# Optimization experiments

Hardware: AMD Instinct MI355X
Metric: run time of the kernel (lower is better)

The kernel has to match this reference:

```python
import jax, jax.numpy as jnp
import numpy as np

EMBED_DIM = 1024
NUM_HEADS = 16
HEAD_DIM = EMBED_DIM // NUM_HEADS
STD = 0.02


def setup_inputs() -> dict:
    key = jax.random.key(0)
    k1, k2, k3 = jax.random.split(key, 3)
    B, S = 2, 2048
    inputs = jax.random.normal(k1, (B, S, EMBED_DIM), dtype=jnp.float32)
    # qkv projection: Linear(E, 3E); torch Linear weight is [out, in]
    w_qkv = jax.random.normal(k2, (3 * EMBED_DIM, EMBED_DIM), dtype=jnp.float32) * STD
    b_qkv = jnp.zeros((3 * EMBED_DIM,), dtype=jnp.float32)
    w_out = jax.random.normal(k3, (EMBED_DIM, EMBED_DIM), dtype=jnp.float32) * STD
    b_out = jnp.zeros((EMBED_DIM,), dtype=jnp.float32)
    return {"inputs": inputs, "w_qkv": w_qkv, "b_qkv": b_qkv, "w_out": w_out, "b_out": b_out}


def reference(inputs, w_qkv, b_qkv, w_out, b_out):
    B, S, E = inputs.shape
    qkv = inputs @ w_qkv.T + b_qkv                      # [B,S,3E]
    q, k, v = jnp.split(qkv, 3, axis=2)                 # each [B,S,E]

    def split_heads(t):
        return t.reshape(B, S, NUM_HEADS, HEAD_DIM).transpose(0, 2, 1, 3)  # [B,H,S,D]

    q, k, v = split_heads(q), split_heads(k), split_heads(v)
    scores = jnp.einsum('bhqd,bhkd->bhqk', q, k) * (1.0 / np.sqrt(HEAD_DIM))
    causal = jnp.tril(jnp.ones((S, S), dtype=bool))     # [S,S]
    scores = jnp.where(causal[None, None, :, :], scores, -jnp.inf)
    probs = jax.nn.softmax(scores, axis=-1)             # dropout is identity in eval mode
    ctx = jnp.einsum('bhqk,bhkd->bhqd', probs, v)       # [B,H,S,D]
    ctx = ctx.transpose(0, 2, 1, 3).reshape(B, S, E)
    return ctx @ w_out.T + b_out
```

## Files before the change

### kernel.cpp

```cpp
#include <hip/hip_runtime.h>
#include <hip/hip_bf16.h>

#define BATCH 2
#define SEQ   2048
#define EMB   1024
#define NHEAD 16
#define HDIM  64
#define MTOT  (BATCH*SEQ)
#define KTOT  EMB

#define NX  (MTOT*EMB)
#define NW1 (3*EMB*EMB)
#define NW2 (EMB*EMB)
#define NCVT (NX+NW1+NW2)

typedef short bf8 __attribute__((ext_vector_type(8)));
typedef short s4v __attribute__((ext_vector_type(4)));
typedef float f4  __attribute__((ext_vector_type(4)));
typedef unsigned int uint;

__device__ __forceinline__ short f2b(float f) {
    __hip_bfloat16 h = __float2bfloat16(f);
    return __builtin_bit_cast(short, h);
}
__device__ __forceinline__ void gl_lds16(const short* g, short* l) {
    __builtin_amdgcn_global_load_lds(
        (const __attribute__((address_space(1))) uint*)g,
        (__attribute__((address_space(3))) uint*)l, 16, 0, 0);
}
#define SWZ_SRC(lane)      ((((lane) ^ ((lane)>>2) ^ ((lane)>>4)) & 3) * 8)
#define SWZ_RD(quad, l16)  ((((quad) ^ (l16) ^ ((l16)>>2)) & 3) * 8)

__global__ __launch_bounds__(256) void cvt_all(
    const float* __restrict__ X, const float* __restrict__ W1,
    const float* __restrict__ W2,
    short* __restrict__ xb, short* __restrict__ w1b, short* __restrict__ w2b)
{
    int i4 = (blockIdx.x * 256 + threadIdx.x) * 4;
    const float* src; short* dst; int off;
    if (i4 < NX)            { src = X;  dst = xb;  off = i4; }
    else if (i4 < NX + NW1) { src = W1; dst = w1b; off = i4 - NX; }
    else                    { src = W2; dst = w2b; off = i4 - NX - NW1; }
    float4 v = *(const float4*)&src[off];
    s4v o; o[0]=f2b(v.x); o[1]=f2b(v.y); o[2]=f2b(v.z); o[3]=f2b(v.w);
    *(s4v*)&dst[off] = o;
}

__global__ __launch_bounds__(256) void gemm_qkv(
    const short* __restrict__ Xb, const short* __restrict__ Wb,
    const float* __restrict__ bias,
    short* __restrict__ qb, short* __restrict__ kb, short* __restrict__ vtb)
{
    __shared__ __align__(16) short As[2*128*32];
    __shared__ __align__(16) short Bs[2*128*32];
    const int tid  = threadIdx.x;
    const int lane = tid & 63;
    const int w    = tid >> 6;
    const int l16  = lane & 15, quad = lane >> 4;
    const int wm   = (w >> 1) * 64, wn = (w & 1) * 64;
    const int srow = (lane >> 2);
    const int scol = SWZ_SRC(lane);

    const int id  = blockIdx.x;
    const int xcd = id & 7, k = id >> 3;
    const int rg  = k / 12, p = k - rg*12;
    const int R   = rg*8 + xcd;
    const int bm  = (R & 7)*4 + (p & 3);
    const int bn  = (R >> 3)*3 + (p >> 2);

    const size_t arow0 = (size_t)(bm*128 + w*32 +  0 + srow)*KTOT + scol;
    const size_t arow1 = (size_t)(bm*128 + w*32 + 16 + srow)*KTOT + scol;
    const size_t brow0 = (size_t)(bn*128 + w*32 +  0 + srow)*KTOT + scol;
    const size_t brow1 = (size_t)(bn*128 + w*32 + 16 + srow)*KTOT + scol;
    const int d0 = (w*32 +  0)*32;
    const int d1 = (w*32 + 16)*32;

    f4 acc[4][4] = {};

    gl_lds16(&Xb[arow0], &As[d0]); gl_lds16(&Xb[arow1], &As[d1]);
    gl_lds16(&Wb[brow0], &Bs[d0]); gl_lds16(&Wb[brow1], &Bs[d1]);
    __syncthreads();

    #pragma unroll 2
    for (int h = 0; h < 32; h++) {
        const int reg = h & 1;
        if (h < 31) {
            const int hn  = h + 1;
            const int off = (hn >> 1)*64 + (hn & 1)*32;
            const int dr  = (hn & 1)*4096;
            gl_lds16(&Xb[arow0 + off], &As[dr + d0]);
            gl_lds16(&Xb[arow1 + off], &As[dr + d1]);
            gl_lds16(&Wb[brow0 + off], &Bs[dr + d0]);
            gl_lds16(&Wb[brow1 + off], &Bs[dr + d1]);
        }
        asm volatile("" ::: "memory");
        bf8 af[4], bf[4];
        #pragma unroll
        for (int t = 0; t < 4; t++) {
            af[t] = *(const bf8*)&As[reg*4096 + (wm + t*16 + l16)*32 + SWZ_RD(quad, l16)];
            bf[t] = *(const bf8*)&Bs[reg*4096 + (wn + t*16 + l16)*32 + SWZ_RD(quad, l16)];
        }
        #pragma unroll
        for (int mt = 0; mt < 4; mt++)
            #pragma unroll
            for (int nt = 0; nt < 4; nt++)
                acc[mt][nt] = __builtin_amdgcn_mfma_f32_16x16x32_bf16(af[mt], bf[nt], acc[mt][nt], 0, 0, 0);
        __syncthreads();
    }
    #pragma unroll
    for (int mt = 0; mt < 4; mt++)
    #pragma unroll
    for (int nt = 0; nt < 4; nt++) {
        int colg = bn*128 + wn + nt*16 + l16;
        float bv = bias[colg];
        #pragma unroll
        for (int r = 0; r < 4; r++) {
            int rowg = bm*128 + wm + mt*16 + quad*4 + r;
            short h = f2b(acc[mt][nt][r] + bv);
            int bb = rowg >> 11, s = rowg & 2047;
            if (colg < 1024) {
                int hh = colg >> 6, d = colg & 63;
                qb[(((bb*NHEAD + hh)*SEQ + s) << 6) + d] = h;
            } else if (colg < 2048) {
                int c2 = colg - 1024, hh = c2 >> 6, d = c2 & 63;
                kb[(((bb*NHEAD + hh)*SEQ + s) << 6) + d] = h;
            } else {
                int c3 = colg - 2048, hh = c3 >> 6, d = c3 & 63;
                int ssw = (s & ~63) | (((s & 15) << 2) | ((s >> 4) & 3));
                vtb[((bb*NHEAD + hh)*HDIM + d)*SEQ + ssw] = h;
            }
        }
    }
}

__global__ __launch_bounds__(256, 3) void attn(
    const short* __restrict__ qb, const short* __restrict__ kb,
    const short* __restrict__ vtb, short* __restrict__ ctx)
{
    __shared__ __align__(16) short Ks[2*4096];
    __shared__ __align__(16) short Vs[2*4096];
    __shared__ __align__(16) short pl[4][32*64];
    const int tid = threadIdx.x;
    const int w = tid >> 6, lane = tid & 63;
    const int l16 = lane & 15, quad = lane >> 4;
    const int f  = blockIdx.x;
    const int xcd = f & 7, j = f >> 3;
    const int bh  = xcd*4 + (j & 3);
    const int slot = j >> 2;
    const int s3 = slot & 7;
    const int hq = slot >> 3;
    const int tq = hq ? (15 - s3) : s3;
    const int q0w = tq*128 + w*16;
    const int base = bh * (SEQ*HDIM);
    short* myp = pl[w];
    const float SC = 0.125f * 1.44269504f;

    const int lq  = lane >> 2;
    const int lsw = SWZ_SRC(lane);

    const bool isk = (w < 2);
    short* tb = isk ? Ks : Vs;
    const int sstep = isk ? 64*HDIM : 64;
    const short* sp0; const short* sp1; const short* sp2; const short* sp3;
    int dof[4];
    {
        const int wb2 = (w & 1) * 4;
        #pragma unroll
        for (int tt = 0; tt < 4; tt++) {
            int t = wb2 + tt, cc = t & 1, g = (t >> 1) & 3;
            dof[tt] = (cc*64 + g*16)*32;
            const short* s = isk ? &kb[base + (g*16 + lq)*HDIM + cc*32 + lsw]
                                 : &vtb[base + (g*16 + lq)*SEQ + cc*32 + lsw];
            if (tt == 0) sp0 = s; else if (tt == 1) sp1 = s;
            else if (tt == 2) sp2 = s; else sp3 = s;
        }
    }

    bf8 qa[2][2];
    #pragma unroll
    for (int rg = 0; rg < 2; rg++)
        #pragma unroll
        for (int kc = 0; kc < 2; kc++)
            qa[rg][kc] = *(const bf8*)&qb[base + (q0w + rg*64 + l16)*HDIM + kc*32 + quad*8];

    f4 oA[4] = {}, oB[4] = {};
    float lacc[2][4] = {};
    const int rdK = l16*32 + SWZ_RD(quad, l16);
    const int nst = 2*tq + 2;

    gl_lds16(sp0, tb + dof[0]); gl_lds16(sp1, tb + dof[1]);
    gl_lds16(sp2, tb + dof[2]); gl_lds16(sp3, tb + dof[3]);
    sp0 += sstep; sp1 += sstep; sp2 += sstep; sp3 += sstep;
    __syncthreads();

    int buf = 0;
    for (int st = 0; st < nst; st++) {
        if (st < nst - 1) {
            short* d = tb + (buf ^ 1)*4096;
            gl_lds16(sp0, d + dof[0]); gl_lds16(sp1, d + dof[1]);
            gl_lds16(sp2, d + dof[2]); gl_lds16(sp3, d + dof[3]);
            sp0 += sstep; sp1 += sstep; sp2 += sstep; sp3 += sstep;
        }
        const int kbase = buf*4096 + rdK;
        const bool rg0act = (st <= 2*tq);
        #pragma unroll
        for (int rg = 0; rg < 2; rg++) {
            if (rg == 0 && !rg0act) continue;
            f4 s[4] = {};
            #pragma unroll
            for (int kf = 0; kf < 4; kf++)
                #pragma unroll
                for (int c = 0; c < 2; c++) {
                    bf8 kfr = *(const bf8*)&Ks[kbase + (c*64 + kf*16)*32];
                    s[kf] = __builtin_amdgcn_mfma_f32_16x16x32_bf16(qa[rg][c], kfr, s[kf], 0, 0, 0);
                }
            const bool diag = (st == 2*tq + rg);
            if (diag) {
                const int j0 = st*64;
                #pragma unroll
                for (int r = 0; r < 4; r++) {
                    const int row = quad*4 + r;
                    const int qi  = q0w + rg*64 + row;
                    float e[4];
                    #pragma unroll
                    for (int kf = 0; kf < 4; kf++) {
                        e[kf] = __builtin_amdgcn_exp2f(s[kf][r] * SC);
                        if (j0 + kf*16 + l16 > qi) e[kf] = 0.0f;
                        lacc[rg][r] += e[kf];
                    }
                    uint u01 = __builtin_amdgcn_perm(__builtin_bit_cast(uint, e[1]),
                                                     __builtin_bit_cast(uint, e[0]), 0x07060302u);
                    uint u23 = __builtin_amdgcn_perm(__builtin_bit_cast(uint, e[3]),
                                                     __builtin_bit_cast(uint, e[2]), 0x07060302u);
                    uint2 pk = {u01, u23};
                    int c8 = ((l16 >> 1) ^ (row & 7));
                    *(uint2*)&myp[(rg*16 + row)*64 + c8*8 + (l16 & 1)*4] = pk;
                }
            } else {
                #pragma unroll
                for (int r = 0; r < 4; r++) {
                    const int row = quad*4 + r;
                    float e[4];
                    #pragma unroll
                    for (int kf = 0; kf < 4; kf++) {
                        e[kf] = __builtin_amdgcn_exp2f(s[kf][r] * SC);
                        lacc[rg][r] += e[kf];
                    }
                    uint u01 = __builtin_amdgcn_perm(__builtin_bit_cast(uint, e[1]),
                                                     __builtin_bit_cast(uint, e[0]), 0x07060302u);
                    uint u23 = __builtin_amdgcn_perm(__builtin_bit_cast(uint, e[3]),
                                                     __builtin_bit_cast(uint, e[2]), 0x07060302u);
                    uint2 pk = {u01, u23};
                    int c8 = ((l16 >> 1) ^ (row & 7));
                    *(uint2*)&myp[(rg*16 + row)*64 + c8*8 + (l16 & 1)*4] = pk;
                }
            }
        }
        asm volatile("" ::: "memory");
        if (rg0act) {
            bf8 pa[2];
            #pragma unroll
            for (int kc = 0; kc < 2; kc++)
                pa[kc] = *(const bf8*)&myp[l16*64 + (((kc*4 + quad) ^ (l16 & 7)))*8];
            #pragma unroll
            for (int dt = 0; dt < 4; dt++)
                #pragma unroll
                for (int c = 0; c < 2; c++) {
                    bf8 vf = *(const bf8*)&Vs[kbase + (c*64 + dt*16)*32];
                    oA[dt] = __builtin_amdgcn_mfma_f32_16x16x32_bf16(pa[c], vf, oA[dt], 0, 0, 0);
                }
        }
        {
            bf8 pa[2];
            #pragma unroll
            for (int kc = 0; kc < 2; kc++)
                pa[kc] = *(const bf8*)&myp[(16 + l16)*64 + (((kc*4 + quad) ^ (l16 & 7)))*8];
            #pragma unroll
            for (int dt = 0; dt < 4; dt++)
                #pragma unroll
                for (int c = 0; c < 2; c++) {
                    bf8 vf = *(const bf8*)&Vs[kbase + (c*64 + dt*16)*32];
                    oB[dt] = __builtin_amdgcn_mfma_f32_16x16x32_bf16(pa[c], vf, oB[dt], 0, 0, 0);
                }
        }
        __syncthreads();
        buf ^= 1;
    }
    #pragma unroll
    for (int rg = 0; rg < 2; rg++)
        #pragma unroll
        for (int r = 0; r < 4; r++) {
            float v = lacc[rg][r];
            v += __shfl_xor(v, 1);
            v += __shfl_xor(v, 2);
            v += __shfl_xor(v, 4);
            v += __shfl_xor(v, 8);
            lacc[rg][r] = v;
        }
    const int b = bh >> 4, h = bh & 15;
    #pragma unroll
    for (int rg = 0; rg < 2; rg++)
        #pragma unroll
        for (int r = 0; r < 4; r++) {
            float inv = 1.0f / lacc[rg][r];
            int qi = q0w + rg*64 + quad*4 + r;
            int rowoff = (b*SEQ + qi)*EMB + h*HDIM;
            #pragma unroll
            for (int dt = 0; dt < 4; dt++)
                ctx[rowoff + dt*16 + l16] = f2b((rg ? oB[dt][r] : oA[dt][r]) * inv);
        }
}

__global__ __launch_bounds__(256) void gemm_out(
    const short* __restrict__ A, const short* __restrict__ Wb,
    const float* __restrict__ bias, float* __restrict__ out)
{
    __shared__ __align__(16) short As[2*128*32];
    __shared__ __align__(16) short Bs[2*64*32];
    const int f = blockIdx.x;
    const int xcd = f & 7, j = f >> 3;
    const int bm  = (xcd & 3)*8 + (j & 7);
    const int bn  = (xcd >> 2)*8 + (j >> 3);
    const int tid  = threadIdx.x;
    const int lane = tid & 63;
    const int w    = tid >> 6;
    const int l16  = lane & 15, quad = lane >> 4;
    const int wm   = (w >> 1) * 64, wn = (w & 1) * 32;
    const int srow = (lane >> 2);
    const int scol = SWZ_SRC(lane);
    f4 acc[4][2] = {};
    for (int k0 = 0; k0 < KTOT; k0 += 64) {
        #pragma unroll
        for (int t = 0; t < 4; t++) {
            const int a  = w*4 + t;
            const int kc = a & 1, g = a >> 1;
            int ra = bm*128 + g*16 + srow;
            gl_lds16(&A[(size_t)ra*KTOT + k0 + kc*32 + scol], &As[kc*4096 + g*16*32]);
        }
        #pragma unroll
        for (int t = 0; t < 2; t++) {
            const int b  = w*2 + t;
            const int kc = b & 1, g = b >> 1;
            int rb = bn*64 + g*16 + srow;
            gl_lds16(&Wb[(size_t)rb*KTOT + k0 + kc*32 + scol], &Bs[kc*2048 + g*16*32]);
        }
        __syncthreads();
        #pragma unroll
        for (int kc = 0; kc < 2; kc++) {
            bf8 af[4], bf[2];
            #pragma unroll
            for (int t = 0; t < 4; t++)
                af[t] = *(const bf8*)&As[kc*4096 + (wm + t*16 + l16)*32 + SWZ_RD(quad, l16)];
            #pragma unroll
            for (int t = 0; t < 2; t++)
                bf[t] = *(const bf8*)&Bs[kc*2048 + (wn + t*16 + l16)*32 + SWZ_RD(quad, l16)];
            #pragma unroll
            for (int mt = 0; mt < 4; mt++)
                #pragma unroll
                for (int nt = 0; nt < 2; nt++)
                    acc[mt][nt] = __builtin_amdgcn_mfma_f32_16x16x32_bf16(af[mt], bf[nt], acc[mt][nt], 0, 0, 0);
        }
        __syncthreads();
    }
    #pragma unroll
    for (int mt = 0; mt < 4; mt++)
    #pragma unroll
    for (int nt = 0; nt < 2; nt++) {
        int colg = bn*64 + wn + nt*16 + l16;
        float bv = bias[colg];
        #pragma unroll
        for (int r = 0; r < 4; r++) {
            int rowg = bm*128 + wm + mt*16 + quad*4 + r;
            out[(size_t)rowg*EMB + colg] = acc[mt][nt][r] + bv;
        }
    }
}

extern "C" void kernel_launch(void* const* d_in, const int* in_sizes, int n_in,
                              void* d_out, int out_size, void* d_ws, size_t ws_size,
                              hipStream_t stream) {
    const float* X    = (const float*)d_in[0];
    const float* Wqkv = (const float*)d_in[1];
    const float* Bqkv = (const float*)d_in[2];
    const float* Wout = (const float*)d_in[3];
    const float* Bout = (const float*)d_in[4];
    float* out = (float*)d_out;

    short* xb    = (short*)d_ws;
    short* w1b   = xb  + NX;
    short* w2b   = w1b + NW1;
    short* qb    = w2b + NW2;
    short* kb    = qb  + NX;
    short* vtb   = kb  + NX;
    short* ctx   = vtb + NX;

    cvt_all<<<NCVT/1024, 256, 0, stream>>>(X, Wqkv, Wout, xb, w1b, w2b);
    gemm_qkv<<<dim3(768), 256, 0, stream>>>(xb, w1b, Bqkv, qb, kb, vtb);
    attn<<<dim3(512), 256, 0, stream>>>(qb, kb, vtb, ctx);
    gemm_out<<<dim3(512), 256, 0, stream>>>(ctx, w2b, Bout, out);
}
```

Before: 173.3 us.

## Triple-buffer QKV GEMM LDS with partial vmcnt waits

Converts the QKV projection GEMM main loop from a double-buffered LDS pipeline to a triple-buffered one. Loads for step h+2 are issued before computing step h. Each barrier waits only until the older group of global-to-LDS loads has landed (vmcnt(4)) instead of draining every outstanding load. This should hide more global memory latency behind MFMA work, at the cost of 50% more LDS per block, which may lower occupancy.

Result: slower. 190.0 us (+9.6%).

```diff
diff --git a/kernel.cpp b/kernel.cpp
--- a/kernel.cpp
+++ b/kernel.cpp
@@ -51,8 +51,8 @@
     const float* __restrict__ bias,
     short* __restrict__ qb, short* __restrict__ kb, short* __restrict__ vtb)
 {
-    __shared__ __align__(16) short As[2*128*32];
-    __shared__ __align__(16) short Bs[2*128*32];
+    __shared__ __align__(16) short As[3*128*32];
+    __shared__ __align__(16) short Bs[3*128*32];
     const int tid  = threadIdx.x;
     const int lane = tid & 63;
     const int w    = tid >> 6;
@@ -74,39 +74,62 @@
     const size_t brow1 = (size_t)(bn*128 + w*32 + 16 + srow)*KTOT + scol;
     const int d0 = (w*32 +  0)*32;
     const int d1 = (w*32 + 16)*32;
+    const int swz = SWZ_RD(quad, l16);
 
     f4 acc[4][4] = {};
 
-    gl_lds16(&Xb[arow0], &As[d0]); gl_lds16(&Xb[arow1], &As[d1]);
-    gl_lds16(&Wb[brow0], &Bs[d0]); gl_lds16(&Wb[brow1], &Bs[d1]);
-    __syncthreads();
-
-    #pragma unroll 2
-    for (int h = 0; h < 32; h++) {
-        const int reg = h & 1;
-        if (h < 31) {
-            const int hn  = h + 1;
-            const int off = (hn >> 1)*64 + (hn & 1)*32;
-            const int dr  = (hn & 1)*4096;
-            gl_lds16(&Xb[arow0 + off], &As[dr + d0]);
-            gl_lds16(&Xb[arow1 + off], &As[dr + d1]);
-            gl_lds16(&Wb[brow0 + off], &Bs[dr + d0]);
-            gl_lds16(&Wb[brow1 + off], &Bs[dr + d1]);
-        }
-        asm volatile("" ::: "memory");
-        bf8 af[4], bf[4];
-        #pragma unroll
-        for (int t = 0; t < 4; t++) {
-            af[t] = *(const bf8*)&As[reg*4096 + (wm + t*16 + l16)*32 + SWZ_RD(quad, l16)];
-            bf[t] = *(const bf8*)&Bs[reg*4096 + (wn + t*16 + l16)*32 + SWZ_RD(quad, l16)];
-        }
-        #pragma unroll
-        for (int mt = 0; mt < 4; mt++)
-            #pragma unroll
-            for (int nt = 0; nt < 4; nt++)
-                acc[mt][nt] = __builtin_amdgcn_mfma_f32_16x16x32_bf16(af[mt], bf[nt], acc[mt][nt], 0, 0, 0);
-        __syncthreads();
-    }
+#define OFFH(hn_) (((hn_) >> 1)*64 + ((hn_) & 1)*32)
+
+#define STAGE_HALF(reg_, off_) do {                                   \
+    const int _dr = (reg_)*4096; const int _o = (off_);               \
+    gl_lds16(&Xb[arow0 + _o], &As[_dr + d0]);                         \
+    gl_lds16(&Xb[arow1 + _o], &As[_dr + d1]);                         \
+    gl_lds16(&Wb[brow0 + _o], &Bs[_dr + d0]);                         \
+    gl_lds16(&Wb[brow1 + _o], &Bs[_dr + d1]);                         \
+} while (0)
+
+#define COMPUTE_HALF(reg_) do {                                       \
+    bf8 af[4], bf[4];                                                 \
+    _Pragma("unroll")                                                 \
+    for (int t = 0; t < 4; t++) {                                     \
+        af[t] = *(const bf8*)&As[(reg_)*4096 + (wm + t*16 + l16)*32 + swz]; \
+        bf[t] = *(const bf8*)&Bs[(reg_)*4096 + (wn + t*16 + l16)*32 + swz]; \
+    }                                                                 \
+    _Pragma("unroll")                                                 \
+    for (int mt = 0; mt < 4; mt++)                                    \
+        _Pragma("unroll")                                             \
+        for (int nt = 0; nt < 4; nt++)                                \
+            acc[mt][nt] = __builtin_amdgcn_mfma_f32_16x16x32_bf16(af[mt], bf[nt], acc[mt][nt], 0, 0, 0); \
+} while (0)
+
+#define BAR4() do { asm volatile("s_waitcnt vmcnt(4)" ::: "memory");  \
+                    __builtin_amdgcn_s_barrier();                     \
+                    asm volatile("" ::: "memory"); } while (0)
+
+    STAGE_HALF(0, 0);
+    STAGE_HALF(1, 32);
+    asm volatile("s_waitcnt vmcnt(4)" ::: "memory");
+    __builtin_amdgcn_s_barrier();
+    asm volatile("" ::: "memory");
+
+    #pragma unroll 1
+    for (int i = 0; i < 10; i++) {
+        const int hb = 3*i;
+        STAGE_HALF(2, OFFH(hb + 2)); COMPUTE_HALF(0); BAR4();
+        STAGE_HALF(0, OFFH(hb + 3)); COMPUTE_HALF(1); BAR4();
+        STAGE_HALF(1, OFFH(hb + 4)); COMPUTE_HALF(2); BAR4();
+    }
+    COMPUTE_HALF(0);
+    asm volatile("s_waitcnt vmcnt(0)" ::: "memory");
+    __builtin_amdgcn_s_barrier();
+    asm volatile("" ::: "memory");
+    COMPUTE_HALF(1);
+
+#undef OFFH
+#undef STAGE_HALF
+#undef COMPUTE_HALF
+#undef BAR4
+
     #pragma unroll
     for (int mt = 0; mt < 4; mt++)
     #pragma unroll
```
